# Optimization experiments

Hardware: AMD Instinct MI355X
Metric: run time of the kernel (lower is better)

## Reference

```python
import jax, jax.numpy as jnp
import numpy as np

NUM_EXPERTS = 8
TOP_K = 2
DIM = 1024
HIDDEN = 2048
TOKENS = 8192


def setup_inputs() -> dict:
    key = jax.random.key(0)
    k0, k1, k2, k3, k4 = jax.random.split(key, 5)
    x = jax.random.normal(k0, (TOKENS, DIM), dtype=jnp.float32)
    gate_w = jax.random.normal(k1, (NUM_EXPERTS, DIM), dtype=jnp.float32) * 0.02
    # SwiGLU expert weights, stacked over experts
    w1 = jax.random.normal(k2, (NUM_EXPERTS, DIM, HIDDEN), dtype=jnp.float32) * 0.02
    w3 = jax.random.normal(k3, (NUM_EXPERTS, DIM, HIDDEN), dtype=jnp.float32) * 0.02
    w2 = jax.random.normal(k4, (NUM_EXPERTS, HIDDEN, DIM), dtype=jnp.float32) * 0.02
    return {"x": x, "gate_w": gate_w, "w1": w1, "w3": w3, "w2": w2}


def reference(x, gate_w, w1, w3, w2):
    # x: [T, D]; gate_w: [E, D]; w1,w3: [E, D, H]; w2: [E, H, D]
    E = gate_w.shape[0]
    gate_logits = x @ gate_w.T                               # [T, E]
    topk_vals, topk_idx = jax.lax.top_k(gate_logits, TOP_K)  # [T, K]
    topk_w = jax.nn.softmax(topk_vals.astype(jnp.float32), axis=-1).astype(x.dtype)
    # per-token per-expert combine weight: sum_k w[t,k] * [sel[t,k]==e]  -> [T, E]
    combine = jnp.einsum('tk,tke->te', topk_w,
                         jax.nn.one_hot(topk_idx, E, dtype=x.dtype))
    # SwiGLU experts, computed per expert over all tokens then masked-combined
    h = jnp.einsum('td,edh->eth', x, w1)                     # [E, T, H]
    g = jnp.einsum('td,edh->eth', x, w3)                     # [E, T, H]
    y = jnp.einsum('eth,ehd->etd', jax.nn.silu(h) * g, w2)   # [E, T, D]
    return jnp.einsum('te,etd->td', combine, y)              # [T, D]
```

## Files before the change

### kernel.cpp

```cpp
#include <hip/hip_runtime.h>
#include <cstdint>
#include <cstddef>

#define T_TOKENS 8192
#define DIM      1024
#define HID      2048
#define NE       8
#define HCAP     17408

typedef __attribute__((ext_vector_type(8))) short short8;
typedef __attribute__((ext_vector_type(4))) float f32x4;

__device__ __forceinline__ unsigned short f2bf(float f) {
  unsigned int u = __builtin_bit_cast(unsigned int, f);
  u += 0x7fffu + ((u >> 16) & 1u);
  return (unsigned short)(u >> 16);
}

__device__ __forceinline__ void gload16(const void* g, void* lds) {
  __builtin_amdgcn_global_load_lds((const __attribute__((address_space(1))) void*)g,
                                   (__attribute__((address_space(3))) void*)lds,
                                   16, 0, 0);
}

__global__ void cvtx_kernel(const float* __restrict__ in, unsigned short* __restrict__ out) {
  size_t i = ((size_t)blockIdx.x * 256 + threadIdx.x) * 8;
  float4 v0 = *(const float4*)(in + i);
  float4 v1 = *(const float4*)(in + i + 4);
  short8 o;
  o[0] = (short)f2bf(v0.x); o[1] = (short)f2bf(v0.y);
  o[2] = (short)f2bf(v0.z); o[3] = (short)f2bf(v0.w);
  o[4] = (short)f2bf(v1.x); o[5] = (short)f2bf(v1.y);
  o[6] = (short)f2bf(v1.z); o[7] = (short)f2bf(v1.w);
  *(short8*)(out + i) = o;
}

__global__ void transcvt_kernel(const float* __restrict__ in, unsigned short* __restrict__ out,
                                int K, int N) {
  __shared__ float tile[64][65];
  int e = blockIdx.z;
  int r  = threadIdx.x >> 2;
  int c0 = (threadIdx.x & 3) * 16;
  const float* src = in + ((size_t)e * K + blockIdx.y * 64 + r) * N + blockIdx.x * 64 + c0;
#pragma unroll
  for (int j = 0; j < 4; j++) {
    float4 v = *(const float4*)(src + j * 4);
    tile[r][c0 + j * 4 + 0] = v.x; tile[r][c0 + j * 4 + 1] = v.y;
    tile[r][c0 + j * 4 + 2] = v.z; tile[r][c0 + j * 4 + 3] = v.w;
  }
  __syncthreads();
  short8 o0, o1;
#pragma unroll
  for (int j = 0; j < 8; j++) o0[j] = (short)f2bf(tile[c0 + j][r]);
#pragma unroll
  for (int j = 0; j < 8; j++) o1[j] = (short)f2bf(tile[c0 + 8 + j][r]);
  unsigned short* dst = out + ((size_t)e * N + blockIdx.x * 64 + r) * K + blockIdx.y * 64 + c0;
  *(short8*)dst = o0;
  *(short8*)(dst + 8) = o1;
}

__global__ void gate_kernel(const float* __restrict__ x, const float* __restrict__ gw,
                            int2* __restrict__ sel, float2* __restrict__ wts) {
  int wid = threadIdx.x >> 6, lane = threadIdx.x & 63;
  int t = blockIdx.x * 4 + wid;
  const float* xr = x + (size_t)t * DIM;
  double acc[NE];
#pragma unroll
  for (int e = 0; e < NE; e++) acc[e] = 0.0;
  for (int i = lane; i < DIM; i += 64) {
    float xv = xr[i];
#pragma unroll
    for (int e = 0; e < NE; e++) acc[e] += (double)xv * (double)gw[e * DIM + i];
  }
#pragma unroll
  for (int e = 0; e < NE; e++) {
    double v = acc[e];
#pragma unroll
    for (int off = 32; off > 0; off >>= 1) v += __shfl_xor(v, off);
    acc[e] = v;
  }
  if (lane == 0) {
    float l[NE];
#pragma unroll
    for (int e = 0; e < NE; e++) l[e] = (float)acc[e];
    int i0 = 0; float v0 = l[0];
#pragma unroll
    for (int e = 1; e < NE; e++) if (l[e] > v0) { v0 = l[e]; i0 = e; }
    int i1 = -1; float v1 = -3.4e38f;
#pragma unroll
    for (int e = 0; e < NE; e++) if (e != i0 && l[e] > v1) { v1 = l[e]; i1 = e; }
    float ew = __expf(v1 - v0);
    float w0 = 1.0f / (1.0f + ew);
    float w1 = ew / (1.0f + ew);
    sel[t] = make_int2(i0, i1);
    wts[t] = make_float2(w0, w1);
  }
}

__global__ void scatter_kernel(const int2* __restrict__ sel, const float2* __restrict__ wts,
                               int* __restrict__ cnt, int* __restrict__ btok,
                               float* __restrict__ bw) {
  __shared__ int hist[NE];
  __shared__ int base[NE];
  int tid = threadIdx.x;
  if (tid < NE) hist[tid] = 0;
  __syncthreads();
  int t = blockIdx.x * 256 + tid;
  int2 s = sel[t]; float2 w = wts[t];
  int p0 = atomicAdd(&hist[s.x], 1);
  int p1 = atomicAdd(&hist[s.y], 1);
  __syncthreads();
  if (tid < NE) base[tid] = atomicAdd(&cnt[tid], hist[tid]);
  __syncthreads();
  int o0 = base[s.x] + p0;
  btok[s.x * T_TOKENS + o0] = t; bw[s.x * T_TOKENS + o0] = w.x;
  int o1 = base[s.y] + p1;
  btok[s.y * T_TOKENS + o1] = t; bw[s.y * T_TOKENS + o1] = w.y;
}

__global__ __launch_bounds__(256, 2) void gemm1_kernel(
    const unsigned short* __restrict__ xb, const unsigned short* __restrict__ w1t,
    const unsigned short* __restrict__ w3t, const int* __restrict__ cnt,
    const int* __restrict__ btok, const unsigned short* __restrict__ zbuf,
    unsigned short* __restrict__ h) {
  int e = blockIdx.z;
  int cn = cnt[e];
  int pc = (cn + 127) & ~127;
  int mt = blockIdx.y;
  if (mt * 128 >= pc) return;
  int hoff = 0;
#pragma unroll
  for (int i = 0; i < NE; i++) { int pi = (cnt[i] + 127) & ~127; if (i < e) hoff += pi; }
  int nt = blockIdx.x;

  __shared__ short8 At8[1024];
  __shared__ short8 B18[512];
  __shared__ short8 B38[512];

  int tid = threadIdx.x, wid = tid >> 6, lane = tid & 63;
  int m0 = mt * 128;

  int swzcol = ((lane & 7) ^ (lane >> 3)) * 8;

  const unsigned short* asrc[4];
#pragma unroll
  for (int rd = 0; rd < 4; rd++) {
    int row = (rd * 4 + wid) * 8 + (lane >> 3);
    int r = m0 + row;
    asrc[rd] = (r < cn) ? (xb + (size_t)btok[e * T_TOKENS + r] * DIM + swzcol)
                        : (zbuf + swzcol);
  }
  const unsigned short* b1s[2]; const unsigned short* b3s[2];
#pragma unroll
  for (int rd = 0; rd < 2; rd++) {
    int row = (rd * 4 + wid) * 8 + (lane >> 3);
    size_t o = ((size_t)e * HID + nt * 64 + row) * DIM + swzcol;
    b1s[rd] = w1t + o; b3s[rd] = w3t + o;
  }

  f32x4 zero = {0.f, 0.f, 0.f, 0.f};
  f32x4 acc1[4][2], acc3[4][2];
#pragma unroll
  for (int m = 0; m < 4; m++)
#pragma unroll
    for (int n = 0; n < 2; n++) { acc1[m][n] = zero; acc3[m][n] = zero; }

  int wr = wid >> 1, wc = wid & 1;
  const char* At = (const char*)At8;
  const char* B1 = (const char*)B18;
  const char* B3 = (const char*)B38;
  int lxor = (lane & 7) << 4;

  for (int kt = 0; kt < DIM / 64; kt++) {
    int ko = kt * 64;
#pragma unroll
    for (int rd = 0; rd < 4; rd++)
      gload16(asrc[rd] + ko, (char*)At8 + (rd * 4 + wid) * 1024);
#pragma unroll
    for (int rd = 0; rd < 2; rd++) {
      gload16(b1s[rd] + ko, (char*)B18 + (rd * 4 + wid) * 1024);
      gload16(b3s[rd] + ko, (char*)B38 + (rd * 4 + wid) * 1024);
    }
    __syncthreads();
#pragma unroll
    for (int ks = 0; ks < 2; ks++) {
      int cb = (ks * 64 + (lane >> 4) * 16) ^ lxor;
      short8 a[4], f1[2], f3[2];
#pragma unroll
      for (int m = 0; m < 4; m++)
        a[m] = *(const short8*)(At + (wr * 64 + m * 16 + (lane & 15)) * 128 + cb);
#pragma unroll
      for (int n = 0; n < 2; n++) {
        int rb = (wc * 32 + n * 16 + (lane & 15)) * 128 + cb;
        f1[n] = *(const short8*)(B1 + rb);
        f3[n] = *(const short8*)(B3 + rb);
      }
#pragma unroll
      for (int m = 0; m < 4; m++)
#pragma unroll
        for (int n = 0; n < 2; n++) {
          acc1[m][n] = __builtin_amdgcn_mfma_f32_16x16x32_bf16(a[m], f1[n], acc1[m][n], 0, 0, 0);
          acc3[m][n] = __builtin_amdgcn_mfma_f32_16x16x32_bf16(a[m], f3[n], acc3[m][n], 0, 0, 0);
        }
    }
    __syncthreads();
  }

#pragma unroll
  for (int m = 0; m < 4; m++)
#pragma unroll
    for (int n = 0; n < 2; n++) {
#pragma unroll
      for (int j = 0; j < 4; j++) {
        float s1 = acc1[m][n][j], s3 = acc3[m][n][j];
        float hv = s1 / (1.0f + __expf(-s1)) * s3;
        int row = wr * 64 + m * 16 + (lane >> 4) * 4 + j;
        int col = nt * 64 + wc * 32 + n * 16 + (lane & 15);
        h[(size_t)(hoff + m0 + row) * HID + col] = f2bf(hv);
      }
    }
}

__global__ __launch_bounds__(256, 2) void gemm2_kernel(
    const unsigned short* __restrict__ h, const unsigned short* __restrict__ w2t,
    const int* __restrict__ cnt, const int* __restrict__ btok,
    const float* __restrict__ bw, float* __restrict__ out) {
  int e = blockIdx.z;
  int cn = cnt[e];
  int pc = (cn + 127) & ~127;
  int mt = blockIdx.y;
  if (mt * 128 >= pc) return;
  int hoff = 0;
#pragma unroll
  for (int i = 0; i < NE; i++) { int pi = (cnt[i] + 127) & ~127; if (i < e) hoff += pi; }
  int nt = blockIdx.x;

  __shared__ short8 At8[1024];
  __shared__ short8 Bt8[1024];

  int tid = threadIdx.x, wid = tid >> 6, lane = tid & 63;
  int m0 = mt * 128;

  int swzcol = ((lane & 7) ^ (lane >> 3)) * 8;

  const unsigned short* as[4]; const unsigned short* bs[4];
#pragma unroll
  for (int rd = 0; rd < 4; rd++) {
    int row = (rd * 4 + wid) * 8 + (lane >> 3);
    as[rd] = h + (size_t)(hoff + m0 + row) * HID + swzcol;
    bs[rd] = w2t + ((size_t)e * DIM + nt * 128 + row) * HID + swzcol;
  }

  f32x4 zero = {0.f, 0.f, 0.f, 0.f};
  f32x4 acc[4][4];
#pragma unroll
  for (int m = 0; m < 4; m++)
#pragma unroll
    for (int n = 0; n < 4; n++) acc[m][n] = zero;

  int wr = wid >> 1, wc = wid & 1;
  const char* At = (const char*)At8;
  const char* Bt = (const char*)Bt8;
  int lxor = (lane & 7) << 4;

  for (int kt = 0; kt < HID / 64; kt++) {
    int ko = kt * 64;
#pragma unroll
    for (int rd = 0; rd < 4; rd++) {
      gload16(as[rd] + ko, (char*)At8 + (rd * 4 + wid) * 1024);
      gload16(bs[rd] + ko, (char*)Bt8 + (rd * 4 + wid) * 1024);
    }
    __syncthreads();
#pragma unroll
    for (int ks = 0; ks < 2; ks++) {
      int cb = (ks * 64 + (lane >> 4) * 16) ^ lxor;
      short8 a[4], b[4];
#pragma unroll
      for (int m = 0; m < 4; m++)
        a[m] = *(const short8*)(At + (wr * 64 + m * 16 + (lane & 15)) * 128 + cb);
#pragma unroll
      for (int n = 0; n < 4; n++)
        b[n] = *(const short8*)(Bt + (wc * 64 + n * 16 + (lane & 15)) * 128 + cb);
#pragma unroll
      for (int m = 0; m < 4; m++)
#pragma unroll
        for (int n = 0; n < 4; n++)
          acc[m][n] = __builtin_amdgcn_mfma_f32_16x16x32_bf16(a[m], b[n], acc[m][n], 0, 0, 0);
    }
    __syncthreads();
  }

#pragma unroll
  for (int m = 0; m < 4; m++)
#pragma unroll
    for (int j = 0; j < 4; j++) {
      int r = m0 + wr * 64 + m * 16 + (lane >> 4) * 4 + j;
      if (r < cn) {
        int t = btok[e * T_TOKENS + r];
        float w = bw[e * T_TOKENS + r];
        size_t ob = (size_t)t * DIM + nt * 128 + wc * 64 + (lane & 15);
#pragma unroll
        for (int n = 0; n < 4; n++)
          atomicAdd(out + ob + n * 16, w * acc[m][n][j]);
      }
    }
}

extern "C" void kernel_launch(void* const* d_in, const int* in_sizes, int n_in,
                              void* d_out, int out_size, void* d_ws, size_t ws_size,
                              hipStream_t stream) {
  const float* x  = (const float*)d_in[0];
  const float* gw = (const float*)d_in[1];
  const float* w1 = (const float*)d_in[2];
  const float* w3 = (const float*)d_in[3];
  const float* w2 = (const float*)d_in[4];
  float* out = (float*)d_out;

  char* ws = (char*)d_ws;
  unsigned short* W1T = (unsigned short*)ws;
  unsigned short* W3T = W1T + (size_t)NE * HID * DIM;
  unsigned short* W2T = W3T + (size_t)NE * HID * DIM;
  unsigned short* XB  = W2T + (size_t)NE * DIM * HID;
  unsigned short* H   = XB + (size_t)T_TOKENS * DIM;
  int*   TOK = (int*)(H + (size_t)HCAP * HID);
  float* BW  = (float*)(TOK + NE * T_TOKENS);
  int*   CNT = (int*)(BW + NE * T_TOKENS);
  unsigned short* ZBUF = (unsigned short*)(CNT + 16);
  int2*   SEL = (int2*)(ZBUF + 1024);
  float2* WTS = (float2*)(SEL + T_TOKENS);

  hipMemsetAsync(d_out, 0, (size_t)out_size * sizeof(float), stream);
  hipMemsetAsync(CNT, 0, 16 * sizeof(int) + 1024 * sizeof(unsigned short), stream);

  cvtx_kernel<<<(T_TOKENS * DIM) / (256 * 8), 256, 0, stream>>>(x, XB);
  transcvt_kernel<<<dim3(HID / 64, DIM / 64, NE), 256, 0, stream>>>(w1, W1T, DIM, HID);
  transcvt_kernel<<<dim3(HID / 64, DIM / 64, NE), 256, 0, stream>>>(w3, W3T, DIM, HID);
  transcvt_kernel<<<dim3(DIM / 64, HID / 64, NE), 256, 0, stream>>>(w2, W2T, HID, DIM);
  gate_kernel<<<T_TOKENS / 4, 256, 0, stream>>>(x, gw, SEL, WTS);
  scatter_kernel<<<T_TOKENS / 256, 256, 0, stream>>>(SEL, WTS, CNT, TOK, BW);
  gemm1_kernel<<<dim3(HID / 64, 64, NE), 256, 0, stream>>>(XB, W1T, W3T, CNT, TOK, ZBUF, H);
  gemm2_kernel<<<dim3(DIM / 128, 64, NE), 256, 0, stream>>>(H, W2T, CNT, TOK, BW, out);
}
```

Baseline: 377.8 us.

## Double-buffer gemm1 with 256x128 tiles, phased barriers, and fuse x conversion into gate

Rewrites the gate/up GEMM to use 512-thread blocks computing 256x128 output tiles. LDS is double-buffered at 128 KB, and the global-to-LDS loads for the next K tile are interleaved across four MFMA phases with explicit vmcnt waits, barriers and setprio. The aim is to hide memory latency behind compute and raise reuse per loaded tile. The bf16 conversion of x moves into the gate kernel, which now reads x with vectorized loads, so one kernel launch and one full read of x go away. The risks are lower occupancy from the large LDS footprint, fragile hand-tuned waitcnt values, and fewer blocks along the token dimension.

New measurement: 392.9 us. +4.0%, slower.

```diff
diff --git a/kernel.cpp b/kernel.cpp
--- a/kernel.cpp
+++ b/kernel.cpp
@@ -9,6 +9,7 @@
 #define HCAP     17408
 
 typedef __attribute__((ext_vector_type(8))) short short8;
+typedef __attribute__((ext_vector_type(4))) short short4v;
 typedef __attribute__((ext_vector_type(4))) float f32x4;
 
 __device__ __forceinline__ unsigned short f2bf(float f) {
@@ -23,17 +24,11 @@
                                    16, 0, 0);
 }
 
-__global__ void cvtx_kernel(const float* __restrict__ in, unsigned short* __restrict__ out) {
-  size_t i = ((size_t)blockIdx.x * 256 + threadIdx.x) * 8;
-  float4 v0 = *(const float4*)(in + i);
-  float4 v1 = *(const float4*)(in + i + 4);
-  short8 o;
-  o[0] = (short)f2bf(v0.x); o[1] = (short)f2bf(v0.y);
-  o[2] = (short)f2bf(v0.z); o[3] = (short)f2bf(v0.w);
-  o[4] = (short)f2bf(v1.x); o[5] = (short)f2bf(v1.y);
-  o[6] = (short)f2bf(v1.z); o[7] = (short)f2bf(v1.w);
-  *(short8*)(out + i) = o;
-}
+#define VMWB(N) do { asm volatile("s_waitcnt vmcnt(" #N ")" ::: "memory"); \
+                     __builtin_amdgcn_s_barrier(); } while (0)
+#define OPENP() do { __builtin_amdgcn_s_barrier(); \
+                     asm volatile("s_waitcnt lgkmcnt(0)" ::: "memory"); \
+                     __builtin_amdgcn_sched_barrier(0); } while (0)
 
 __global__ void transcvt_kernel(const float* __restrict__ in, unsigned short* __restrict__ out,
                                 int K, int N) {
@@ -60,17 +55,29 @@
 }
 
 __global__ void gate_kernel(const float* __restrict__ x, const float* __restrict__ gw,
-                            int2* __restrict__ sel, float2* __restrict__ wts) {
+                            int2* __restrict__ sel, float2* __restrict__ wts,
+                            unsigned short* __restrict__ xb) {
   int wid = threadIdx.x >> 6, lane = threadIdx.x & 63;
   int t = blockIdx.x * 4 + wid;
   const float* xr = x + (size_t)t * DIM;
+  unsigned short* xo = xb + (size_t)t * DIM;
   double acc[NE];
 #pragma unroll
   for (int e = 0; e < NE; e++) acc[e] = 0.0;
-  for (int i = lane; i < DIM; i += 64) {
-    float xv = xr[i];
-#pragma unroll
-    for (int e = 0; e < NE; e++) acc[e] += (double)xv * (double)gw[e * DIM + i];
+#pragma unroll
+  for (int p = 0; p < 4; p++) {
+    int idx = p * 256 + lane * 4;
+    float4 xv = *(const float4*)(xr + idx);
+    short4v o;
+    o[0] = (short)f2bf(xv.x); o[1] = (short)f2bf(xv.y);
+    o[2] = (short)f2bf(xv.z); o[3] = (short)f2bf(xv.w);
+    *(short4v*)(xo + idx) = o;
+#pragma unroll
+    for (int e = 0; e < NE; e++) {
+      float4 g = *(const float4*)(gw + e * DIM + idx);
+      acc[e] += (double)xv.x * (double)g.x + (double)xv.y * (double)g.y
+              + (double)xv.z * (double)g.z + (double)xv.w * (double)g.w;
+    }
   }
 #pragma unroll
   for (int e = 0; e < NE; e++) {
@@ -118,7 +125,7 @@
   btok[s.y * T_TOKENS + o1] = t; bw[s.y * T_TOKENS + o1] = w.y;
 }
 
-__global__ __launch_bounds__(256, 2) void gemm1_kernel(
+__global__ __launch_bounds__(512, 2) void gemm1_kernel(
     const unsigned short* __restrict__ xb, const unsigned short* __restrict__ w1t,
     const unsigned short* __restrict__ w3t, const int* __restrict__ cnt,
     const int* __restrict__ btok, const unsigned short* __restrict__ zbuf,
@@ -127,98 +134,155 @@
   int cn = cnt[e];
   int pc = (cn + 127) & ~127;
   int mt = blockIdx.y;
-  if (mt * 128 >= pc) return;
+  if (mt * 256 >= pc) return;
   int hoff = 0;
 #pragma unroll
   for (int i = 0; i < NE; i++) { int pi = (cnt[i] + 127) & ~127; if (i < e) hoff += pi; }
   int nt = blockIdx.x;
 
-  __shared__ short8 At8[1024];
-  __shared__ short8 B18[512];
-  __shared__ short8 B38[512];
+  __shared__ short8 ldsbuf[8192];
+  char* lds = (char*)ldsbuf;
 
   int tid = threadIdx.x, wid = tid >> 6, lane = tid & 63;
-  int m0 = mt * 128;
-
-  int swzcol = ((lane & 7) ^ (lane >> 3)) * 8;
-
+  int m0 = mt * 256;
+  int wr = wid >> 2, wc = wid & 3;
+  int l15 = lane & 15;
+
+  int s = wid * 8 + (lane >> 3);
+  int swzcol = ((lane & 7) ^ ((lane >> 3) & 7)) * 8;
   const unsigned short* asrc[4];
 #pragma unroll
   for (int rd = 0; rd < 4; rd++) {
-    int row = (rd * 4 + wid) * 8 + (lane >> 3);
-    int r = m0 + row;
+    int r = m0 + rd * 64 + s;
     asrc[rd] = (r < cn) ? (xb + (size_t)btok[e * T_TOKENS + r] * DIM + swzcol)
                         : (zbuf + swzcol);
   }
-  const unsigned short* b1s[2]; const unsigned short* b3s[2];
+  const unsigned short* b1src[2]; const unsigned short* b3src[2];
 #pragma unroll
   for (int rd = 0; rd < 2; rd++) {
-    int row = (rd * 4 + wid) * 8 + (lane >> 3);
-    size_t o = ((size_t)e * HID + nt * 64 + row) * DIM + swzcol;
-    b1s[rd] = w1t + o; b3s[rd] = w3t + o;
-  }
+    size_t o = ((size_t)e * HID + nt * 128 + rd * 64 + s) * DIM + swzcol;
+    b1src[rd] = w1t + o; b3src[rd] = w3t + o;
+  }
+  int ldst = wid * 1024;
+
+  int cb0 = ((lane >> 4) * 16) ^ ((lane & 7) << 4);
+  int cb1 = (64 + (lane >> 4) * 16) ^ ((lane & 7) << 4);
+  int offA  = wr * 8192 + l15 * 128;
+  int offB1 = 32768 + wc * 4096 + l15 * 128;
+  int offB3 = 49152 + wc * 4096 + l15 * 128;
 
   f32x4 zero = {0.f, 0.f, 0.f, 0.f};
-  f32x4 acc1[4][2], acc3[4][2];
-#pragma unroll
-  for (int m = 0; m < 4; m++)
+  f32x4 acc1[8][2], acc3[8][2];
+#pragma unroll
+  for (int m = 0; m < 8; m++)
 #pragma unroll
     for (int n = 0; n < 2; n++) { acc1[m][n] = zero; acc3[m][n] = zero; }
-
-  int wr = wid >> 1, wc = wid & 1;
-  const char* At = (const char*)At8;
-  const char* B1 = (const char*)B18;
-  const char* B3 = (const char*)B38;
-  int lxor = (lane & 7) << 4;
-
-  for (int kt = 0; kt < DIM / 64; kt++) {
-    int ko = kt * 64;
-#pragma unroll
-    for (int rd = 0; rd < 4; rd++)
-      gload16(asrc[rd] + ko, (char*)At8 + (rd * 4 + wid) * 1024);
-#pragma unroll
-    for (int rd = 0; rd < 2; rd++) {
-      gload16(b1s[rd] + ko, (char*)B18 + (rd * 4 + wid) * 1024);
-      gload16(b3s[rd] + ko, (char*)B38 + (rd * 4 + wid) * 1024);
-    }
-    __syncthreads();
-#pragma unroll
-    for (int ks = 0; ks < 2; ks++) {
-      int cb = (ks * 64 + (lane >> 4) * 16) ^ lxor;
-      short8 a[4], f1[2], f3[2];
-#pragma unroll
-      for (int m = 0; m < 4; m++)
-        a[m] = *(const short8*)(At + (wr * 64 + m * 16 + (lane & 15)) * 128 + cb);
-#pragma unroll
-      for (int n = 0; n < 2; n++) {
-        int rb = (wc * 32 + n * 16 + (lane & 15)) * 128 + cb;
-        f1[n] = *(const short8*)(B1 + rb);
-        f3[n] = *(const short8*)(B3 + rb);
-      }
-#pragma unroll
-      for (int m = 0; m < 4; m++)
-#pragma unroll
-        for (int n = 0; n < 2; n++) {
-          acc1[m][n] = __builtin_amdgcn_mfma_f32_16x16x32_bf16(a[m], f1[n], acc1[m][n], 0, 0, 0);
-          acc3[m][n] = __builtin_amdgcn_mfma_f32_16x16x32_bf16(a[m], f3[n], acc3[m][n], 0, 0, 0);
-        }
-    }
-    __syncthreads();
-  }
-
-#pragma unroll
-  for (int m = 0; m < 4; m++)
-#pragma unroll
-    for (int n = 0; n < 2; n++) {
+  short8 af[4][2], f1[2][2], f3[2][2];
+
+#define S_A0 gload16(asrc[0] + ko, nb + ldst);           gload16(asrc[2] + ko, nb + 8192 + ldst)
+#define S_A1 gload16(asrc[1] + ko, nb + 16384 + ldst);   gload16(asrc[3] + ko, nb + 24576 + ldst)
+#define S_B1 gload16(b1src[0] + ko, nb + 32768 + ldst);  gload16(b1src[1] + ko, nb + 40960 + ldst)
+#define S_B3 gload16(b3src[0] + ko, nb + 49152 + ldst);  gload16(b3src[1] + ko, nb + 57344 + ldst)
+
+#define STEP1(CUR, NB, KO, STG, W0, W1, W2, W3)                                  \
+  {                                                                              \
+    const char* cu = (CUR); char* nb = (NB); int ko = (KO);                      \
+    (void)nb; (void)ko;                                                          \
+                                          \
+    _Pragma("unroll") for (int mm = 0; mm < 4; mm++) {                           \
+      af[mm][0] = *(const short8*)(cu + offA + mm * 2048 + cb0);                 \
+      af[mm][1] = *(const short8*)(cu + offA + mm * 2048 + cb1);                 \
+    }                                                                            \
+    _Pragma("unroll") for (int nn = 0; nn < 2; nn++) {                           \
+      f1[nn][0] = *(const short8*)(cu + offB1 + nn * 2048 + cb0);                \
+      f1[nn][1] = *(const short8*)(cu + offB1 + nn * 2048 + cb1);                \
+    }                                                                            \
+    if (STG) { S_A0; }                                                           \
+    OPENP();                                                                     \
+    __builtin_amdgcn_s_setprio(1);                                               \
+    _Pragma("unroll") for (int mm = 0; mm < 4; mm++)                             \
+      _Pragma("unroll") for (int nn = 0; nn < 2; nn++) {                         \
+        acc1[mm][nn] = __builtin_amdgcn_mfma_f32_16x16x32_bf16(af[mm][0], f1[nn][0], acc1[mm][nn], 0, 0, 0); \
+        acc1[mm][nn] = __builtin_amdgcn_mfma_f32_16x16x32_bf16(af[mm][1], f1[nn][1], acc1[mm][nn], 0, 0, 0); \
+      }                                                                          \
+    __builtin_amdgcn_s_setprio(0);                                               \
+    VMWB(W0);                                                                    \
+                                                    \
+    _Pragma("unroll") for (int nn = 0; nn < 2; nn++) {                           \
+      f3[nn][0] = *(const short8*)(cu + offB3 + nn * 2048 + cb0);                \
+      f3[nn][1] = *(const short8*)(cu + offB3 + nn * 2048 + cb1);                \
+    }                                                                            \
+    if (STG) { S_B1; }                                                           \
+    OPENP();                                                                     \
+    __builtin_amdgcn_s_setprio(1);                                               \
+    _Pragma("unroll") for (int mm = 0; mm < 4; mm++)                             \
+      _Pragma("unroll") for (int nn = 0; nn < 2; nn++) {                         \
+        acc3[mm][nn] = __builtin_amdgcn_mfma_f32_16x16x32_bf16(af[mm][0], f3[nn][0], acc3[mm][nn], 0, 0, 0); \
+        acc3[mm][nn] = __builtin_amdgcn_mfma_f32_16x16x32_bf16(af[mm][1], f3[nn][1], acc3[mm][nn], 0, 0, 0); \
+      }                                                                          \
+    __builtin_amdgcn_s_setprio(0);                                               \
+    VMWB(W1);                                                                    \
+                                \
+    _Pragma("unroll") for (int mm = 0; mm < 4; mm++) {                           \
+      af[mm][0] = *(const short8*)(cu + 16384 + offA + mm * 2048 + cb0);         \
+      af[mm][1] = *(const short8*)(cu + 16384 + offA + mm * 2048 + cb1);         \
+    }                                                                            \
+    if (STG) { S_B3; }                                                           \
+    OPENP();                                                                     \
+    __builtin_amdgcn_s_setprio(1);                                               \
+    _Pragma("unroll") for (int mm = 0; mm < 4; mm++)                             \
+      _Pragma("unroll") for (int nn = 0; nn < 2; nn++) {                         \
+        acc1[4 + mm][nn] = __builtin_amdgcn_mfma_f32_16x16x32_bf16(af[mm][0], f1[nn][0], acc1[4 + mm][nn], 0, 0, 0); \
+        acc1[4 + mm][nn] = __builtin_amdgcn_mfma_f32_16x16x32_bf16(af[mm][1], f1[nn][1], acc1[4 + mm][nn], 0, 0, 0); \
+      }                                                                          \
+    __builtin_amdgcn_s_setprio(0);                                               \
+    VMWB(W2);                                                                    \
+                                                             \
+    if (STG) { S_A1; }                                                           \
+    OPENP();                                                                     \
+    __builtin_amdgcn_s_setprio(1);                                               \
+    _Pragma("unroll") for (int mm = 0; mm < 4; mm++)                             \
+      _Pragma("unroll") for (int nn = 0; nn < 2; nn++) {                         \
+        acc3[4 + mm][nn] = __builtin_amdgcn_mfma_f32_16x16x32_bf16(af[mm][0], f3[nn][0], acc3[4 + mm][nn], 0, 0, 0); \
+        acc3[4 + mm][nn] = __builtin_amdgcn_mfma_f32_16x16x32_bf16(af[mm][1], f3[nn][1], acc3[4 + mm][nn], 0, 0, 0); \
+      }                                                                          \
+    __builtin_amdgcn_s_setprio(0);                                               \
+    VMWB(W3);                                                                    \
+  }
+
+  {
+    char* nb = lds; int ko = 0;
+    S_A0; S_B1; S_B3; S_A1;
+  }
+  VMWB(4);
+
+#pragma unroll 1
+  for (int kt = 0; kt < 14; kt += 2) {
+    int ko0 = (kt + 1) * 64;
+    STEP1(lds, lds + 65536, ko0, true, 4, 4, 6, 4);
+    STEP1(lds + 65536, lds, ko0 + 64, true, 4, 4, 6, 4);
+  }
+  STEP1(lds, lds + 65536, 15 * 64, true, 4, 4, 6, 4);
+  STEP1(lds + 65536, lds, 0, false, 2, 0, 0, 0);
+
+#pragma unroll
+  for (int m = 0; m < 8; m++)
+#pragma unroll
+    for (int n = 0; n < 2; n++)
 #pragma unroll
       for (int j = 0; j < 4; j++) {
         float s1 = acc1[m][n][j], s3 = acc3[m][n][j];
         float hv = s1 / (1.0f + __expf(-s1)) * s3;
-        int row = wr * 64 + m * 16 + (lane >> 4) * 4 + j;
-        int col = nt * 64 + wc * 32 + n * 16 + (lane & 15);
-        h[(size_t)(hoff + m0 + row) * HID + col] = f2bf(hv);
+        int row = wr * 128 + m * 16 + (lane >> 4) * 4 + j;
+        if (m0 + row < pc) {
+          int col = nt * 128 + wc * 32 + n * 16 + l15;
+          h[(size_t)(hoff + m0 + row) * HID + col] = f2bf(hv);
+        }
       }
-    }
+#undef S_A0
+#undef S_A1
+#undef S_B1
+#undef S_B3
 }
 
 __global__ __launch_bounds__(256, 2) void gemm2_kernel(
@@ -332,12 +396,11 @@
   hipMemsetAsync(d_out, 0, (size_t)out_size * sizeof(float), stream);
   hipMemsetAsync(CNT, 0, 16 * sizeof(int) + 1024 * sizeof(unsigned short), stream);
 
-  cvtx_kernel<<<(T_TOKENS * DIM) / (256 * 8), 256, 0, stream>>>(x, XB);
+  gate_kernel<<<T_TOKENS / 4, 256, 0, stream>>>(x, gw, SEL, WTS, XB);
+  scatter_kernel<<<T_TOKENS / 256, 256, 0, stream>>>(SEL, WTS, CNT, TOK, BW);
   transcvt_kernel<<<dim3(HID / 64, DIM / 64, NE), 256, 0, stream>>>(w1, W1T, DIM, HID);
   transcvt_kernel<<<dim3(HID / 64, DIM / 64, NE), 256, 0, stream>>>(w3, W3T, DIM, HID);
   transcvt_kernel<<<dim3(DIM / 64, HID / 64, NE), 256, 0, stream>>>(w2, W2T, HID, DIM);
-  gate_kernel<<<T_TOKENS / 4, 256, 0, stream>>>(x, gw, SEL, WTS);
-  scatter_kernel<<<T_TOKENS / 256, 256, 0, stream>>>(SEL, WTS, CNT, TOK, BW);
-  gemm1_kernel<<<dim3(HID / 64, 64, NE), 256, 0, stream>>>(XB, W1T, W3T, CNT, TOK, ZBUF, H);
+  gemm1_kernel<<<dim3(HID / 128, 32, NE), 512, 0, stream>>>(XB, W1T, W3T, CNT, TOK, ZBUF, H);
   gemm2_kernel<<<dim3(DIM / 128, 64, NE), 256, 0, stream>>>(H, W2T, CNT, TOK, BW, out);
 }
```

## Fuse x bf16 conversion into gate kernel and remap GEMM grids across XCDs

Applied to the files above, without the earlier changes.

Removes the standalone x-to-bf16 conversion kernel and does that conversion inside the gate kernel, which already reads x, now with float4 loads. Both expert GEMMs switch to a 1D grid whose block index is remapped so consecutive blocks go to different XCD-interleaved chunks. Within a chunk, tiles of the same expert and N-column sit together, which should improve L2 reuse of the weight tiles. Early-exit blocks for empty M tiles are still launched, and the gate kernel now does extra work, which may lengthen it.

After: 377.3 us. No clear change (-0.1%).

```diff
diff --git a/kernel.cpp b/kernel.cpp
--- a/kernel.cpp
+++ b/kernel.cpp
@@ -9,6 +9,7 @@
 #define HCAP     17408
 
 typedef __attribute__((ext_vector_type(8))) short short8;
+typedef __attribute__((ext_vector_type(4))) short short4v;
 typedef __attribute__((ext_vector_type(4))) float f32x4;
 
 __device__ __forceinline__ unsigned short f2bf(float f) {
@@ -21,18 +22,6 @@
   __builtin_amdgcn_global_load_lds((const __attribute__((address_space(1))) void*)g,
                                    (__attribute__((address_space(3))) void*)lds,
                                    16, 0, 0);
-}
-
-__global__ void cvtx_kernel(const float* __restrict__ in, unsigned short* __restrict__ out) {
-  size_t i = ((size_t)blockIdx.x * 256 + threadIdx.x) * 8;
-  float4 v0 = *(const float4*)(in + i);
-  float4 v1 = *(const float4*)(in + i + 4);
-  short8 o;
-  o[0] = (short)f2bf(v0.x); o[1] = (short)f2bf(v0.y);
-  o[2] = (short)f2bf(v0.z); o[3] = (short)f2bf(v0.w);
-  o[4] = (short)f2bf(v1.x); o[5] = (short)f2bf(v1.y);
-  o[6] = (short)f2bf(v1.z); o[7] = (short)f2bf(v1.w);
-  *(short8*)(out + i) = o;
 }
 
 __global__ void transcvt_kernel(const float* __restrict__ in, unsigned short* __restrict__ out,
@@ -60,17 +49,29 @@
 }
 
 __global__ void gate_kernel(const float* __restrict__ x, const float* __restrict__ gw,
-                            int2* __restrict__ sel, float2* __restrict__ wts) {
+                            int2* __restrict__ sel, float2* __restrict__ wts,
+                            unsigned short* __restrict__ xb) {
   int wid = threadIdx.x >> 6, lane = threadIdx.x & 63;
   int t = blockIdx.x * 4 + wid;
   const float* xr = x + (size_t)t * DIM;
+  unsigned short* xo = xb + (size_t)t * DIM;
   double acc[NE];
 #pragma unroll
   for (int e = 0; e < NE; e++) acc[e] = 0.0;
-  for (int i = lane; i < DIM; i += 64) {
-    float xv = xr[i];
-#pragma unroll
-    for (int e = 0; e < NE; e++) acc[e] += (double)xv * (double)gw[e * DIM + i];
+#pragma unroll
+  for (int p = 0; p < 4; p++) {
+    int idx = p * 256 + lane * 4;
+    float4 xv = *(const float4*)(xr + idx);
+    short4v o;
+    o[0] = (short)f2bf(xv.x); o[1] = (short)f2bf(xv.y);
+    o[2] = (short)f2bf(xv.z); o[3] = (short)f2bf(xv.w);
+    *(short4v*)(xo + idx) = o;
+#pragma unroll
+    for (int e = 0; e < NE; e++) {
+      float4 g = *(const float4*)(gw + e * DIM + idx);
+      acc[e] += (double)xv.x * (double)g.x + (double)xv.y * (double)g.y
+              + (double)xv.z * (double)g.z + (double)xv.w * (double)g.w;
+    }
   }
 #pragma unroll
   for (int e = 0; e < NE; e++) {
@@ -118,20 +119,27 @@
   btok[s.y * T_TOKENS + o1] = t; bw[s.y * T_TOKENS + o1] = w.y;
 }
 
+#define G1_NT (HID / 64)
+#define G1_MT 64
+#define G1_NWG (G1_NT * G1_MT * NE)
 __global__ __launch_bounds__(256, 2) void gemm1_kernel(
     const unsigned short* __restrict__ xb, const unsigned short* __restrict__ w1t,
     const unsigned short* __restrict__ w3t, const int* __restrict__ cnt,
     const int* __restrict__ btok, const unsigned short* __restrict__ zbuf,
     unsigned short* __restrict__ h) {
-  int e = blockIdx.z;
+  int bid = blockIdx.x;
+  int wg = (bid & 7) * (G1_NWG / 8) + (bid >> 3);
+  int e  = wg / (G1_NT * G1_MT);
+  int rem = wg % (G1_NT * G1_MT);
+  int nt = rem / G1_MT;
+  int mt = rem % G1_MT;
+
   int cn = cnt[e];
   int pc = (cn + 127) & ~127;
-  int mt = blockIdx.y;
   if (mt * 128 >= pc) return;
   int hoff = 0;
 #pragma unroll
   for (int i = 0; i < NE; i++) { int pi = (cnt[i] + 127) & ~127; if (i < e) hoff += pi; }
-  int nt = blockIdx.x;
 
   __shared__ short8 At8[1024];
   __shared__ short8 B18[512];
@@ -221,19 +229,26 @@
     }
 }
 
+#define G2_NT (DIM / 128)
+#define G2_MT 64
+#define G2_NWG (G2_NT * G2_MT * NE)
 __global__ __launch_bounds__(256, 2) void gemm2_kernel(
     const unsigned short* __restrict__ h, const unsigned short* __restrict__ w2t,
     const int* __restrict__ cnt, const int* __restrict__ btok,
     const float* __restrict__ bw, float* __restrict__ out) {
-  int e = blockIdx.z;
+  int bid = blockIdx.x;
+  int wg = (bid & 7) * (G2_NWG / 8) + (bid >> 3);
+  int e  = wg / (G2_NT * G2_MT);
+  int rem = wg % (G2_NT * G2_MT);
+  int nt = rem / G2_MT;
+  int mt = rem % G2_MT;
+
   int cn = cnt[e];
   int pc = (cn + 127) & ~127;
-  int mt = blockIdx.y;
   if (mt * 128 >= pc) return;
   int hoff = 0;
 #pragma unroll
   for (int i = 0; i < NE; i++) { int pi = (cnt[i] + 127) & ~127; if (i < e) hoff += pi; }
-  int nt = blockIdx.x;
 
   __shared__ short8 At8[1024];
   __shared__ short8 Bt8[1024];
@@ -332,12 +347,11 @@
   hipMemsetAsync(d_out, 0, (size_t)out_size * sizeof(float), stream);
   hipMemsetAsync(CNT, 0, 16 * sizeof(int) + 1024 * sizeof(unsigned short), stream);
 
-  cvtx_kernel<<<(T_TOKENS * DIM) / (256 * 8), 256, 0, stream>>>(x, XB);
+  gate_kernel<<<T_TOKENS / 4, 256, 0, stream>>>(x, gw, SEL, WTS, XB);
+  scatter_kernel<<<T_TOKENS / 256, 256, 0, stream>>>(SEL, WTS, CNT, TOK, BW);
   transcvt_kernel<<<dim3(HID / 64, DIM / 64, NE), 256, 0, stream>>>(w1, W1T, DIM, HID);
   transcvt_kernel<<<dim3(HID / 64, DIM / 64, NE), 256, 0, stream>>>(w3, W3T, DIM, HID);
   transcvt_kernel<<<dim3(DIM / 64, HID / 64, NE), 256, 0, stream>>>(w2, W2T, HID, DIM);
-  gate_kernel<<<T_TOKENS / 4, 256, 0, stream>>>(x, gw, SEL, WTS);
-  scatter_kernel<<<T_TOKENS / 256, 256, 0, stream>>>(SEL, WTS, CNT, TOK, BW);
-  gemm1_kernel<<<dim3(HID / 64, 64, NE), 256, 0, stream>>>(XB, W1T, W3T, CNT, TOK, ZBUF, H);
-  gemm2_kernel<<<dim3(DIM / 128, 64, NE), 256, 0, stream>>>(H, W2T, CNT, TOK, BW, out);
-}
+  gemm1_kernel<<<G1_NWG, 256, 0, stream>>>(XB, W1T, W3T, CNT, TOK, ZBUF, H);
+  gemm2_kernel<<<G2_NWG, 256, 0, stream>>>(H, W2T, CNT, TOK, BW, out);
+}
```
